# Optimization experiments

Measured on AMD Instinct MI355X. Metric: run time of the kernel, lower is better.

Reference implementation:

```python
import jax, jax.numpy as jnp
import numpy as np

N_KNOTS = 4
OUT_DIM = 512
IN_DIM = 512
BATCH = 4096


def setup_inputs() -> dict:
    key = jax.random.key(0)
    k1, k2, k3 = jax.random.split(key, 3)
    # inputs: [B, IN_DIM + N_KNOTS]; last N_KNOTS cols are phase blend weights
    x = jax.random.normal(k1, (BATCH, IN_DIM + N_KNOTS), dtype=jnp.float32)
    # make the phase columns a valid convex-ish blend (softmax), as in PFNN usage
    phase = jax.nn.softmax(x[:, -N_KNOTS:], axis=-1)
    x = jnp.concatenate([x[:, :-N_KNOTS], phase], axis=-1)
    bound = np.sqrt(6.0 / (OUT_DIM * IN_DIM))
    weight_knots = jax.random.uniform(k2, (N_KNOTS, OUT_DIM, IN_DIM), dtype=jnp.float32,
                                      minval=-bound, maxval=bound)
    bias_knots = jnp.zeros((N_KNOTS, OUT_DIM), dtype=jnp.float32)
    return {"inputs": x, "weight_knots": weight_knots, "bias_knots": bias_knots}


def reference(inputs, weight_knots, bias_knots):
    # Split features and phase blend coefficients
    p = inputs[:, -N_KNOTS:]          # [B, K]
    feat = inputs[:, :-N_KNOTS]       # [B, IN]
    # Original: wi = sum_k p[:,k] * W[k]  ([B,out,in]); res = wi @ feat + bi.
    # Fused equivalent: contract W with feat first, then blend over knots,
    # avoiding the [B,out,in] intermediate.
    # knot_out: [B, K, OUT]
    knot_out = jnp.einsum('koi,bi->bko', weight_knots, feat)
    res = jnp.einsum('bk,bko->bo', p, knot_out) + p @ bias_knots  # [B, OUT]
    res = jax.nn.elu(res)
    return res
```

## Files before the change

### kernel.cpp

```cpp
#include <hip/hip_runtime.h>

#define BATCH 4096
#define IN_DIM 512
#define OUT_DIM 512
#define NK 4
#define SX (IN_DIM + NK)
#define BM 64
#define BN 64
#define BK 64
#define KT (IN_DIM / BK)

typedef short bf16x8 __attribute__((ext_vector_type(8)));
typedef float f32x4 __attribute__((ext_vector_type(4)));

__device__ __forceinline__ unsigned short f2bf(float f) {
    unsigned int u = __float_as_uint(f);
    u = u + 0x7FFFu + ((u >> 16) & 1u);
    return (unsigned short)(u >> 16);
}

__device__ __forceinline__ void gload_lds16(const void* g, void* l) {
    __builtin_amdgcn_global_load_lds(
        (const __attribute__((address_space(1))) void*)g,
        (__attribute__((address_space(3))) void*)l, 16, 0, 0);
}

__global__ __launch_bounds__(256) void convert_kernel(
    const float* __restrict__ x, const float* __restrict__ w,
    unsigned short* __restrict__ wb, unsigned short* __restrict__ fb)
{
    const int WCH = NK * OUT_DIM * IN_DIM / 4;
    int g = blockIdx.x * 256 + threadIdx.x;
    if (g < WCH) {
        const float4 v = reinterpret_cast<const float4*>(w)[g];
        unsigned short h[4] = {f2bf(v.x), f2bf(v.y), f2bf(v.z), f2bf(v.w)};
        *reinterpret_cast<uint2*>(&wb[g * 4]) = *reinterpret_cast<const uint2*>(h);
    } else {
        int idx = g - WCH;
        int row = idx >> 7;
        int c   = (idx & 127) * 4;
        const float4 v = *reinterpret_cast<const float4*>(&x[(size_t)row * SX + c]);
        unsigned short h[4] = {f2bf(v.x), f2bf(v.y), f2bf(v.z), f2bf(v.w)};
        *reinterpret_cast<uint2*>(&fb[row * IN_DIM + c]) = *reinterpret_cast<const uint2*>(h);
    }
}

__global__ __launch_bounds__(256) void mpl_gemm(
    const unsigned short* __restrict__ fb,
    const unsigned short* __restrict__ wb,
    const float* __restrict__ x,
    const float* __restrict__ bias,
    float* __restrict__ out)
{
    __shared__ unsigned short As[2 * BM * BK];
    __shared__ unsigned short Bs[2 * NK * BN * BK];

    const int tid  = threadIdx.x;
    const int lane = tid & 63;
    const int wid  = tid >> 6;
    const int wr   = (wid >> 1) * 32;
    const int wc   = (wid & 1) * 32;
    const int R0   = blockIdx.x * BM;
    const int C0   = blockIdx.y * BN;

    f32x4 acc[NK][2][2] = {};
    const int cl = lane & 15;
    const int kb = (lane >> 4) * 8;

    auto stage = [&](int b, int k0) {
        #pragma unroll
        for (int j = 0; j < 2; ++j) {
            int ch  = j * 256 + tid;
            int row = ch >> 3;
            int c   = ch & 7;
            gload_lds16(fb + (size_t)(R0 + row) * IN_DIM + k0 + ((c ^ (row & 7)) << 3),
                        &As[b * BM * BK + ch * 8]);
        }
        #pragma unroll
        for (int j = 0; j < 8; ++j) {
            int ch  = j * 256 + tid;
            int kn  = ch >> 9;
            int rem = ch & 511;
            int row = rem >> 3;
            int c   = rem & 7;
            gload_lds16(wb + (size_t)kn * OUT_DIM * IN_DIM + (size_t)(C0 + row) * IN_DIM
                           + k0 + ((c ^ (row & 7)) << 3),
                        &Bs[b * NK * BN * BK + ch * 8]);
        }
    };

    auto compute = [&](int b) {
        const char* Ab = reinterpret_cast<const char*>(As) + b * BM * BK * 2;
        const char* Bb = reinterpret_cast<const char*>(Bs) + b * NK * BN * BK * 2;
        #pragma unroll
        for (int kk = 0; kk < BK; kk += 32) {
            bf16x8 af[2];
            #pragma unroll
            for (int m = 0; m < 2; ++m) {
                int row  = wr + m * 16 + cl;
                int boff = (row * 128 + (kk + kb) * 2) ^ ((row & 7) << 4);
                af[m] = *reinterpret_cast<const bf16x8*>(Ab + boff);
            }
            #pragma unroll
            for (int kn = 0; kn < NK; ++kn) {
                bf16x8 bfr[2];
                #pragma unroll
                for (int n = 0; n < 2; ++n) {
                    int row  = wc + n * 16 + cl;
                    int boff = (row * 128 + (kk + kb) * 2) ^ ((row & 7) << 4);
                    bfr[n] = *reinterpret_cast<const bf16x8*>(Bb + kn * 8192 + boff);
                }
                __builtin_amdgcn_s_setprio(1);
                #pragma unroll
                for (int m = 0; m < 2; ++m)
                    #pragma unroll
                    for (int n = 0; n < 2; ++n)
                        acc[kn][m][n] = __builtin_amdgcn_mfma_f32_16x16x32_bf16(
                            af[m], bfr[n], acc[kn][m][n], 0, 0, 0);
                __builtin_amdgcn_s_setprio(0);
            }
        }
    };

    stage(0, 0);
    stage(1, BK);
    #pragma unroll
    for (int kt = 0; kt < KT; ++kt) {
        const int cur = kt & 1;
        if (kt < KT - 1) asm volatile("s_waitcnt vmcnt(10)" ::: "memory");
        else             asm volatile("s_waitcnt vmcnt(0)"  ::: "memory");
        __builtin_amdgcn_s_barrier();
        compute(cur);
        __builtin_amdgcn_s_barrier();
        if (kt < KT - 2) stage(cur, (kt + 2) * BK);
    }

    const int rl = (lane >> 4) * 4;
    float bcol[2][NK];
    #pragma unroll
    for (int n = 0; n < 2; ++n)
        #pragma unroll
        for (int k = 0; k < NK; ++k)
            bcol[n][k] = bias[k * OUT_DIM + C0 + wc + n * 16 + cl];

    #pragma unroll
    for (int m = 0; m < 2; ++m) {
        #pragma unroll
        for (int r = 0; r < 4; ++r) {
            const int row = R0 + wr + m * 16 + rl + r;
            const float4 p = *reinterpret_cast<const float4*>(&x[(size_t)row * SX + IN_DIM]);
            const float pk[4] = {p.x, p.y, p.z, p.w};
            #pragma unroll
            for (int n = 0; n < 2; ++n) {
                float v = 0.f;
                #pragma unroll
                for (int k = 0; k < NK; ++k)
                    v += pk[k] * (acc[k][m][n][r] + bcol[n][k]);
                v = (v > 0.f) ? v : expm1f(v);
                out[(size_t)row * OUT_DIM + C0 + wc + n * 16 + cl] = v;
            }
        }
    }
}

#define LDT 72
__global__ __launch_bounds__(256) void mpl_kernel_fb(
    const float* __restrict__ x, const float* __restrict__ w,
    const float* __restrict__ bias, float* __restrict__ out)
{
    __shared__ unsigned short Asf[BM][LDT];
    __shared__ unsigned short Bsf[NK][64][LDT];
    const int tid = threadIdx.x, lane = tid & 63, wid = tid >> 6;
    const int wr = (wid >> 1) * 32, wc = (wid & 1) * 32;
    const int R0 = blockIdx.x * BM, C0 = blockIdx.y * 64;
    f32x4 acc[NK][2][2] = {};
    const int cl = lane & 15, kb = (lane >> 4) * 8;
    for (int kt = 0; kt < KT; ++kt) {
        const int k0 = kt * BK;
        __syncthreads();
        #pragma unroll
        for (int j = 0; j < 4; ++j) {
            int f = tid + 256 * j, row = f >> 4, c4 = (f & 15) * 4;
            const float4 v = *reinterpret_cast<const float4*>(&x[(size_t)(R0 + row) * SX + k0 + c4]);
            unsigned short h[4] = {f2bf(v.x), f2bf(v.y), f2bf(v.z), f2bf(v.w)};
            *reinterpret_cast<uint2*>(&Asf[row][c4]) = *reinterpret_cast<const uint2*>(h);
        }
        #pragma unroll
        for (int kn = 0; kn < NK; ++kn)
            #pragma unroll
            for (int j = 0; j < 4; ++j) {
                int f = tid + 256 * j, row = f >> 4, c4 = (f & 15) * 4;
                const float4 v = *reinterpret_cast<const float4*>(
                    &w[(size_t)kn * OUT_DIM * IN_DIM + (size_t)(C0 + row) * IN_DIM + k0 + c4]);
                unsigned short h[4] = {f2bf(v.x), f2bf(v.y), f2bf(v.z), f2bf(v.w)};
                *reinterpret_cast<uint2*>(&Bsf[kn][row][c4]) = *reinterpret_cast<const uint2*>(h);
            }
        __syncthreads();
        #pragma unroll
        for (int kk = 0; kk < BK; kk += 32) {
            bf16x8 af[2];
            #pragma unroll
            for (int m = 0; m < 2; ++m)
                af[m] = *reinterpret_cast<const bf16x8*>(&Asf[wr + m * 16 + cl][kk + kb]);
            #pragma unroll
            for (int kn = 0; kn < NK; ++kn) {
                bf16x8 bfr[2];
                #pragma unroll
                for (int n = 0; n < 2; ++n)
                    bfr[n] = *reinterpret_cast<const bf16x8*>(&Bsf[kn][wc + n * 16 + cl][kk + kb]);
                #pragma unroll
                for (int m = 0; m < 2; ++m)
                    #pragma unroll
                    for (int n = 0; n < 2; ++n)
                        acc[kn][m][n] = __builtin_amdgcn_mfma_f32_16x16x32_bf16(
                            af[m], bfr[n], acc[kn][m][n], 0, 0, 0);
            }
        }
    }
    const int rl = (lane >> 4) * 4;
    float bcol[2][NK];
    #pragma unroll
    for (int n = 0; n < 2; ++n)
        #pragma unroll
        for (int k = 0; k < NK; ++k)
            bcol[n][k] = bias[k * OUT_DIM + C0 + wc + n * 16 + cl];
    #pragma unroll
    for (int m = 0; m < 2; ++m)
        #pragma unroll
        for (int r = 0; r < 4; ++r) {
            const int row = R0 + wr + m * 16 + rl + r;
            const float4 p = *reinterpret_cast<const float4*>(&x[(size_t)row * SX + IN_DIM]);
            const float pk[4] = {p.x, p.y, p.z, p.w};
            #pragma unroll
            for (int n = 0; n < 2; ++n) {
                float v = 0.f;
                #pragma unroll
                for (int k = 0; k < NK; ++k)
                    v += pk[k] * (acc[k][m][n][r] + bcol[n][k]);
                v = (v > 0.f) ? v : expm1f(v);
                out[(size_t)row * OUT_DIM + C0 + wc + n * 16 + cl] = v;
            }
        }
}

extern "C" void kernel_launch(void* const* d_in, const int* in_sizes, int n_in,
                              void* d_out, int out_size, void* d_ws, size_t ws_size,
                              hipStream_t stream) {
    const float* x    = (const float*)d_in[0];
    const float* w    = (const float*)d_in[1];
    const float* bias = (const float*)d_in[2];
    float* out        = (float*)d_out;

    const size_t wb_bytes = (size_t)NK * OUT_DIM * IN_DIM * 2;
    const size_t fb_bytes = (size_t)BATCH * IN_DIM * 2;

    if (ws_size < wb_bytes + fb_bytes) {
        dim3 grid(BATCH / BM, OUT_DIM / 64);
        mpl_kernel_fb<<<grid, dim3(256), 0, stream>>>(x, w, bias, out);
        return;
    }

    unsigned short* wb = (unsigned short*)d_ws;
    unsigned short* fb = (unsigned short*)((char*)d_ws + wb_bytes);

    const int total_chunks = NK * OUT_DIM * IN_DIM / 4 + BATCH * IN_DIM / 4;
    convert_kernel<<<dim3(total_chunks / 256), dim3(256), 0, stream>>>(x, w, wb, fb);

    dim3 grid(BATCH / BM, OUT_DIM / BN);
    mpl_gemm<<<grid, dim3(256), 0, stream>>>(fb, wb, x, bias, out);
}
```

Before: 26.56 us.

## Halve K tile and use slab-major LDS layout to raise GEMM occupancy

The main GEMM kernel now uses a 32-wide K tile. LDS is stored slab-major (each 8-element K chunk is contiguous across rows), which replaces the XOR swizzle, and the wait count is adjusted to the smaller number of loads per stage. Launch bounds request 4 blocks per SM, since the LDS footprint is halved, which should improve occupancy and latency hiding. In exchange there are twice as many K iterations and barriers, and the main loop is no longer unrolled.

```diff
diff --git a/kernel.cpp b/kernel.cpp
--- a/kernel.cpp
+++ b/kernel.cpp
@@ -7,8 +7,8 @@
 #define SX (IN_DIM + NK)
 #define BM 64
 #define BN 64
-#define BK 64
-#define KT (IN_DIM / BK)
+#define BK 32
+#define KT2 (IN_DIM / BK)
 
 typedef short bf16x8 __attribute__((ext_vector_type(8)));
 typedef float f32x4 __attribute__((ext_vector_type(4)));
@@ -45,7 +45,7 @@
     }
 }
 
-__global__ __launch_bounds__(256) void mpl_gemm(
+__global__ __launch_bounds__(256, 4) void mpl_gemm(
     const unsigned short* __restrict__ fb,
     const unsigned short* __restrict__ wb,
     const float* __restrict__ x,
@@ -64,75 +64,62 @@
     const int C0   = blockIdx.y * BN;
 
     f32x4 acc[NK][2][2] = {};
-    const int cl = lane & 15;
-    const int kb = (lane >> 4) * 8;
+    const int cl    = lane & 15;
+    const int cslab = lane >> 4;
 
     auto stage = [&](int b, int k0) {
-        #pragma unroll
-        for (int j = 0; j < 2; ++j) {
-            int ch  = j * 256 + tid;
-            int row = ch >> 3;
-            int c   = ch & 7;
-            gload_lds16(fb + (size_t)(R0 + row) * IN_DIM + k0 + ((c ^ (row & 7)) << 3),
-                        &As[b * BM * BK + ch * 8]);
-        }
-        #pragma unroll
-        for (int j = 0; j < 8; ++j) {
-            int ch  = j * 256 + tid;
-            int kn  = ch >> 9;
-            int rem = ch & 511;
-            int row = rem >> 3;
-            int c   = rem & 7;
-            gload_lds16(wb + (size_t)kn * OUT_DIM * IN_DIM + (size_t)(C0 + row) * IN_DIM
-                           + k0 + ((c ^ (row & 7)) << 3),
-                        &Bs[b * NK * BN * BK + ch * 8]);
+        {
+            int row = tid & 63;
+            int c   = tid >> 6;
+            gload_lds16(fb + (size_t)(R0 + row) * IN_DIM + k0 + c * 8,
+                        &As[b * BM * BK + tid * 8]);
+        }
+        #pragma unroll
+        for (int kn = 0; kn < NK; ++kn) {
+            int col = tid & 63;
+            int c   = tid >> 6;
+            gload_lds16(wb + (size_t)kn * OUT_DIM * IN_DIM + (size_t)(C0 + col) * IN_DIM
+                           + k0 + c * 8,
+                        &Bs[b * NK * BN * BK + (kn * 256 + tid) * 8]);
         }
     };
 
     auto compute = [&](int b) {
-        const char* Ab = reinterpret_cast<const char*>(As) + b * BM * BK * 2;
-        const char* Bb = reinterpret_cast<const char*>(Bs) + b * NK * BN * BK * 2;
-        #pragma unroll
-        for (int kk = 0; kk < BK; kk += 32) {
-            bf16x8 af[2];
-            #pragma unroll
-            for (int m = 0; m < 2; ++m) {
-                int row  = wr + m * 16 + cl;
-                int boff = (row * 128 + (kk + kb) * 2) ^ ((row & 7) << 4);
-                af[m] = *reinterpret_cast<const bf16x8*>(Ab + boff);
-            }
-            #pragma unroll
-            for (int kn = 0; kn < NK; ++kn) {
-                bf16x8 bfr[2];
-                #pragma unroll
-                for (int n = 0; n < 2; ++n) {
-                    int row  = wc + n * 16 + cl;
-                    int boff = (row * 128 + (kk + kb) * 2) ^ ((row & 7) << 4);
-                    bfr[n] = *reinterpret_cast<const bf16x8*>(Bb + kn * 8192 + boff);
-                }
-                __builtin_amdgcn_s_setprio(1);
-                #pragma unroll
-                for (int m = 0; m < 2; ++m)
-                    #pragma unroll
-                    for (int n = 0; n < 2; ++n)
-                        acc[kn][m][n] = __builtin_amdgcn_mfma_f32_16x16x32_bf16(
-                            af[m], bfr[n], acc[kn][m][n], 0, 0, 0);
-                __builtin_amdgcn_s_setprio(0);
-            }
+        const unsigned short* Ab = As + b * BM * BK;
+        const unsigned short* Bb = Bs + b * NK * BN * BK;
+        bf16x8 af[2];
+        #pragma unroll
+        for (int m = 0; m < 2; ++m)
+            af[m] = *reinterpret_cast<const bf16x8*>(
+                &Ab[cslab * 512 + (wr + m * 16 + cl) * 8]);
+        #pragma unroll
+        for (int kn = 0; kn < NK; ++kn) {
+            bf16x8 bfr[2];
+            #pragma unroll
+            for (int n = 0; n < 2; ++n)
+                bfr[n] = *reinterpret_cast<const bf16x8*>(
+                    &Bb[kn * 2048 + cslab * 512 + (wc + n * 16 + cl) * 8]);
+            __builtin_amdgcn_s_setprio(1);
+            #pragma unroll
+            for (int m = 0; m < 2; ++m)
+                #pragma unroll
+                for (int n = 0; n < 2; ++n)
+                    acc[kn][m][n] = __builtin_amdgcn_mfma_f32_16x16x32_bf16(
+                        af[m], bfr[n], acc[kn][m][n], 0, 0, 0);
+            __builtin_amdgcn_s_setprio(0);
         }
     };
 
     stage(0, 0);
     stage(1, BK);
-    #pragma unroll
-    for (int kt = 0; kt < KT; ++kt) {
+    for (int kt = 0; kt < KT2; ++kt) {
         const int cur = kt & 1;
-        if (kt < KT - 1) asm volatile("s_waitcnt vmcnt(10)" ::: "memory");
-        else             asm volatile("s_waitcnt vmcnt(0)"  ::: "memory");
+        if (kt < KT2 - 1) asm volatile("s_waitcnt vmcnt(5)" ::: "memory");
+        else              asm volatile("s_waitcnt vmcnt(0)" ::: "memory");
         __builtin_amdgcn_s_barrier();
         compute(cur);
         __builtin_amdgcn_s_barrier();
-        if (kt < KT - 2) stage(cur, (kt + 2) * BK);
+        if (kt < KT2 - 2) stage(cur, (kt + 2) * BK);
     }
 
     const int rl = (lane >> 4) * 4;
@@ -175,8 +162,8 @@
     const int R0 = blockIdx.x * BM, C0 = blockIdx.y * 64;
     f32x4 acc[NK][2][2] = {};
     const int cl = lane & 15, kb = (lane >> 4) * 8;
-    for (int kt = 0; kt < KT; ++kt) {
-        const int k0 = kt * BK;
+    for (int kt = 0; kt < IN_DIM / 64; ++kt) {
+        const int k0 = kt * 64;
         __syncthreads();
         #pragma unroll
         for (int j = 0; j < 4; ++j) {
@@ -197,7 +184,7 @@
             }
         __syncthreads();
         #pragma unroll
-        for (int kk = 0; kk < BK; kk += 32) {
+        for (int kk = 0; kk < 64; kk += 32) {
             bf16x8 af[2];
             #pragma unroll
             for (int m = 0; m < 2; ++m)
```

Result: slower. 36.63 us (+37.9%).

## Fuse fp32-to-bf16 feature conversion into GEMM A-tile load path

Applied to the files above, without the earlier changes.

Removes the separate conversion of the input features to bf16 in the pre-pass. The GEMM now loads fp32 features into registers, converts them, and writes them to swizzled LDS, software-pipelined one tile ahead. This drops a global write and re-read of the bf16 feature copy. In exchange it adds register pressure and VALU conversion work inside the GEMM, and the fp32 features are reconverted by every column block.

```diff
diff --git a/kernel.cpp b/kernel.cpp
--- a/kernel.cpp
+++ b/kernel.cpp
@@ -26,27 +26,15 @@
 }
 
 __global__ __launch_bounds__(256) void convert_kernel(
-    const float* __restrict__ x, const float* __restrict__ w,
-    unsigned short* __restrict__ wb, unsigned short* __restrict__ fb)
+    const float* __restrict__ w, unsigned short* __restrict__ wb)
 {
-    const int WCH = NK * OUT_DIM * IN_DIM / 4;
     int g = blockIdx.x * 256 + threadIdx.x;
-    if (g < WCH) {
-        const float4 v = reinterpret_cast<const float4*>(w)[g];
-        unsigned short h[4] = {f2bf(v.x), f2bf(v.y), f2bf(v.z), f2bf(v.w)};
-        *reinterpret_cast<uint2*>(&wb[g * 4]) = *reinterpret_cast<const uint2*>(h);
-    } else {
-        int idx = g - WCH;
-        int row = idx >> 7;
-        int c   = (idx & 127) * 4;
-        const float4 v = *reinterpret_cast<const float4*>(&x[(size_t)row * SX + c]);
-        unsigned short h[4] = {f2bf(v.x), f2bf(v.y), f2bf(v.z), f2bf(v.w)};
-        *reinterpret_cast<uint2*>(&fb[row * IN_DIM + c]) = *reinterpret_cast<const uint2*>(h);
-    }
+    const float4 v = reinterpret_cast<const float4*>(w)[g];
+    unsigned short h[4] = {f2bf(v.x), f2bf(v.y), f2bf(v.z), f2bf(v.w)};
+    *reinterpret_cast<uint2*>(&wb[g * 4]) = *reinterpret_cast<const uint2*>(h);
 }
 
 __global__ __launch_bounds__(256) void mpl_gemm(
-    const unsigned short* __restrict__ fb,
     const unsigned short* __restrict__ wb,
     const float* __restrict__ x,
     const float* __restrict__ bias,
@@ -67,15 +55,12 @@
     const int cl = lane & 15;
     const int kb = (lane >> 4) * 8;
 
-    auto stage = [&](int b, int k0) {
-        #pragma unroll
-        for (int j = 0; j < 2; ++j) {
-            int ch  = j * 256 + tid;
-            int row = ch >> 3;
-            int c   = ch & 7;
-            gload_lds16(fb + (size_t)(R0 + row) * IN_DIM + k0 + ((c ^ (row & 7)) << 3),
-                        &As[b * BM * BK + ch * 8]);
-        }
+    const int arow = tid >> 2;
+    const int akq  = tid & 3;
+
+    float4 areg[2][4];
+
+    auto BSTAGE = [&](int b, int k0) {
         #pragma unroll
         for (int j = 0; j < 8; ++j) {
             int ch  = j * 256 + tid;
@@ -88,6 +73,27 @@
                         &Bs[b * NK * BN * BK + ch * 8]);
         }
     };
+    auto ALOAD = [&](int pa, int ktile) {
+        #pragma unroll
+        for (int j = 0; j < 4; ++j)
+            areg[pa][j] = *reinterpret_cast<const float4*>(
+                &x[(size_t)(R0 + arow) * SX + ktile * BK + akq * 16 + j * 4]);
+    };
+    auto AWRITE = [&](int pa, int b) {
+        unsigned short h[16];
+        #pragma unroll
+        for (int j = 0; j < 4; ++j) {
+            h[j * 4 + 0] = f2bf(areg[pa][j].x);
+            h[j * 4 + 1] = f2bf(areg[pa][j].y);
+            h[j * 4 + 2] = f2bf(areg[pa][j].z);
+            h[j * 4 + 3] = f2bf(areg[pa][j].w);
+        }
+        char* base = reinterpret_cast<char*>(As) + b * 8192;
+        int o0 = (arow * 128 + akq * 32)      ^ ((arow & 7) << 4);
+        int o1 = (arow * 128 + akq * 32 + 16) ^ ((arow & 7) << 4);
+        *reinterpret_cast<bf16x8*>(base + o0) = *reinterpret_cast<const bf16x8*>(&h[0]);
+        *reinterpret_cast<bf16x8*>(base + o1) = *reinterpret_cast<const bf16x8*>(&h[8]);
+    };
 
     auto compute = [&](int b) {
         const char* Ab = reinterpret_cast<const char*>(As) + b * BM * BK * 2;
@@ -122,17 +128,28 @@
         }
     };
 
-    stage(0, 0);
-    stage(1, BK);
-    #pragma unroll
+    ALOAD(0, 0);
+    BSTAGE(0, 0);
+    BSTAGE(1, BK);
+    asm volatile("s_waitcnt vmcnt(16)" ::: "memory");
+    AWRITE(0, 0);
+    ALOAD(1, 1);
+
     for (int kt = 0; kt < KT; ++kt) {
         const int cur = kt & 1;
-        if (kt < KT - 1) asm volatile("s_waitcnt vmcnt(10)" ::: "memory");
+        if (kt < KT - 1) asm volatile("s_waitcnt vmcnt(12)" ::: "memory");
         else             asm volatile("s_waitcnt vmcnt(0)"  ::: "memory");
+        asm volatile("s_waitcnt lgkmcnt(0)" ::: "memory");
         __builtin_amdgcn_s_barrier();
         compute(cur);
         __builtin_amdgcn_s_barrier();
-        if (kt < KT - 2) stage(cur, (kt + 2) * BK);
+        if (kt + 2 < KT) BSTAGE(cur, (kt + 2) * BK);
+        if (kt + 1 < KT) {
+            if (kt + 2 < KT) asm volatile("s_waitcnt vmcnt(8)" ::: "memory");
+            else             asm volatile("s_waitcnt vmcnt(0)" ::: "memory");
+            if ((kt + 1) & 1) AWRITE(1, 1); else AWRITE(0, 0);
+            if (kt + 2 < KT) { if (kt & 1) ALOAD(1, kt + 2); else ALOAD(0, kt + 2); }
+        }
     }
 
     const int rl = (lane >> 4) * 4;
@@ -252,20 +269,17 @@
     float* out        = (float*)d_out;
 
     const size_t wb_bytes = (size_t)NK * OUT_DIM * IN_DIM * 2;
-    const size_t fb_bytes = (size_t)BATCH * IN_DIM * 2;
-
-    if (ws_size < wb_bytes + fb_bytes) {
+
+    if (ws_size < wb_bytes) {
         dim3 grid(BATCH / BM, OUT_DIM / 64);
         mpl_kernel_fb<<<grid, dim3(256), 0, stream>>>(x, w, bias, out);
         return;
     }
 
     unsigned short* wb = (unsigned short*)d_ws;
-    unsigned short* fb = (unsigned short*)((char*)d_ws + wb_bytes);
-
-    const int total_chunks = NK * OUT_DIM * IN_DIM / 4 + BATCH * IN_DIM / 4;
-    convert_kernel<<<dim3(total_chunks / 256), dim3(256), 0, stream>>>(x, w, wb, fb);
+
+    convert_kernel<<<dim3(NK * OUT_DIM * IN_DIM / 4 / 256), dim3(256), 0, stream>>>(w, wb);
 
     dim3 grid(BATCH / BM, OUT_DIM / BN);
-    mpl_gemm<<<grid, dim3(256), 0, stream>>>(fb, wb, x, bias, out);
-}
+    mpl_gemm<<<grid, dim3(256), 0, stream>>>(wb, x, bias, out);
+}
```

New measurement: 29.30 us. 10.3% more time.
